# Kernel tuning notes

Hardware: AMD Instinct MI355X
Metric: run time of the kernel (lower is better)

Reference implementation:

```python
import jax, jax.numpy as jnp
import numpy as np

B, D, K, V = 8192, 64, 200, 100000
EPS = 1e-5


def setup_inputs() -> dict:
    key = jax.random.key(0)
    ks = jax.random.split(key, 16)
    n = lambda k, s, sc=1.0: jax.random.normal(k, s, dtype=jnp.float32) * sc
    sw = 0.05  # weight scale for numeric stability
    inp = {
        'v_embed': n(ks[0], (V, D)),
        'embeds_u_1': n(ks[1], (B, D)),
        'embeds_u_2': n(ks[2], (B, D)),
        'embeds_u_3': n(ks[3], (B, D)),
        'embeds_u_4': n(ks[4], (B, D)),
        'embeds_v': n(ks[5], (B, D)),
        'w_ur1_w': n(ks[6], (D, D), sw), 'w_ur1_b': jnp.zeros((D,), jnp.float32),
        'w_ur2_w': n(ks[7], (D, D), sw), 'w_ur2_b': jnp.zeros((D,), jnp.float32),
        'w_vr1_w': n(ks[8], (D, D), sw), 'w_vr1_b': jnp.zeros((D,), jnp.float32),
        'w_vr2_w': n(ks[9], (D, D), sw), 'w_vr2_b': jnp.zeros((D,), jnp.float32),
        'w_uv1_w': n(ks[10], (2 * D, D), sw), 'w_uv1_b': jnp.zeros((D,), jnp.float32),
        'w_uv2_w': n(ks[11], (D, 16), sw), 'w_uv2_b': jnp.zeros((16,), jnp.float32),
        'w_uv3_w': n(ks[12], (16, 1), sw), 'w_uv3_b': jnp.zeros((1,), jnp.float32),
        'nodes_v': jax.random.randint(ks[13], (B,), 0, V),
        'nbr_idx': jax.random.randint(ks[14], (B, K), 0, V),
        'nbr_len': jax.random.randint(ks[15], (B,), 1, K),
    }
    for name, dim in (('bn1', D), ('bn2', D), ('bn3', D), ('bn4', 16)):
        inp[name + '_g'] = jnp.ones((dim,), jnp.float32)
        inp[name + '_b'] = jnp.zeros((dim,), jnp.float32)
        inp[name + '_m'] = jnp.zeros((dim,), jnp.float32)
        inp[name + '_v'] = jnp.ones((dim,), jnp.float32)
    return inp


def _bn(x, g, b, m, v):
    return (x - m) * jax.lax.rsqrt(v + EPS) * g + b


def reference(v_embed, embeds_u_1, embeds_u_2, embeds_u_3, embeds_u_4, embeds_v,
              w_ur1_w, w_ur1_b, w_ur2_w, w_ur2_b,
              w_vr1_w, w_vr1_b, w_vr2_w, w_vr2_b,
              w_uv1_w, w_uv1_b, w_uv2_w, w_uv2_b, w_uv3_w, w_uv3_b,
              bn1_g, bn1_b, bn1_m, bn1_v,
              bn2_g, bn2_b, bn2_m, bn2_v,
              bn3_g, bn3_b, bn3_m, bn3_v,
              bn4_g, bn4_b, bn4_m, bn4_v,
              nodes_v, nbr_idx, nbr_len):
    sg = jax.lax.stop_gradient
    # ragged nearest-neighbor min distance (torch used .data -> detached)
    ve = sg(v_embed)
    new_v = ve[nodes_v]                                    # [B, D]
    nbr = ve[nbr_idx]                                      # [B, K, D]
    d = jnp.sqrt(jnp.sum((new_v[:, None, :] - nbr) ** 2, axis=-1))  # [B, K]
    kk = nbr_idx.shape[1]
    mask = jnp.arange(kk)[None, :] < jnp.maximum(nbr_len, 1)[:, None]
    d_min = jnp.min(jnp.where(mask, d, jnp.inf), axis=1)   # [B]
    # per-sample curiosity c_u (detached in torch via .data)
    dist = lambda a, b: jnp.sqrt(jnp.sum((a - b) ** 2, axis=-1))
    u1, u2, u3, u4 = sg(embeds_u_1), sg(embeds_u_2), sg(embeds_u_3), sg(embeds_u_4)
    c = (dist(u1, u2) + dist(u2, u3) + dist(u3, u4)) / 3.0  # [B]
    # exponential-decay fusion of temporal user embeddings: e^-4..e^-1 / sum
    w = jnp.exp(-jnp.arange(4, 0, -1, dtype=jnp.float32))
    w = w / jnp.sum(w)
    embeds_u = (embeds_u_1 * w[0] + embeds_u_2 * w[1]
                + embeds_u_3 * w[2] + embeds_u_4 * w[3])
    # MLP head (eval mode: BN with running stats, dropout off)
    x_u = jax.nn.relu(_bn(embeds_u @ w_ur1_w + w_ur1_b, bn1_g, bn1_b, bn1_m, bn1_v))
    x_u = x_u @ w_ur2_w + w_ur2_b
    x_v = jax.nn.relu(_bn(embeds_v @ w_vr1_w + w_vr1_b, bn2_g, bn2_b, bn2_m, bn2_v))
    x_v = x_v @ w_vr2_w + w_vr2_b
    x = jnp.concatenate([x_u, x_v], axis=1)                # [B, 2D]
    x = jax.nn.relu(_bn(x @ w_uv1_w + w_uv1_b, bn3_g, bn3_b, bn3_m, bn3_v))
    x = jax.nn.relu(_bn(x @ w_uv2_w + w_uv2_b, bn4_g, bn4_b, bn4_m, bn4_v))
    scores = (x @ w_uv3_w + w_uv3_b)[:, 0]                 # [B]
    # unexpectedness term: batch min-max normalize, 6t*exp(-6t)
    t = (d_min - jnp.min(d_min)) / (jnp.max(d_min) - jnp.min(d_min))
    unexp = 6.0 * t * jnp.exp(-6.0 * t)
    cn = (c - jnp.min(c)) / (jnp.max(c) - jnp.min(c))
    return scores + unexp * cn
```

## Files before the change

kernel.cpp:

```cpp
#include <hip/hip_runtime.h>
#include <math.h>

#define NROWS 8192
#define DIM 64
#define KNBR 200
#define NSLICE 8
#define SLICE_ROWS 12500
#define RPB 32
#define BN_EPS 1e-5f
#define BIGF 3.402823466e38f


__device__ __forceinline__ float matvec64(const float* xlds,
                                          const float* __restrict__ W,
                                          int lane) {
    float acc = 0.f;
#pragma unroll
    for (int i4 = 0; i4 < 16; ++i4) {
        float4 xv = *(const float4*)(xlds + i4 * 4);
        acc = fmaf(xv.x, W[(i4 * 4 + 0) * 64 + lane], acc);
        acc = fmaf(xv.y, W[(i4 * 4 + 1) * 64 + lane], acc);
        acc = fmaf(xv.z, W[(i4 * 4 + 2) * 64 + lane], acc);
        acc = fmaf(xv.w, W[(i4 * 4 + 3) * 64 + lane], acc);
    }
    return acc;
}

__device__ __forceinline__ float matvec128(const float* xlds,
                                           const float* __restrict__ W,
                                           int lane) {
    float acc = 0.f;
#pragma unroll
    for (int i4 = 0; i4 < 32; ++i4) {
        float4 xv = *(const float4*)(xlds + i4 * 4);
        acc = fmaf(xv.x, W[(i4 * 4 + 0) * 64 + lane], acc);
        acc = fmaf(xv.y, W[(i4 * 4 + 1) * 64 + lane], acc);
        acc = fmaf(xv.z, W[(i4 * 4 + 2) * 64 + lane], acc);
        acc = fmaf(xv.w, W[(i4 * 4 + 3) * 64 + lane], acc);
    }
    return acc;
}

__device__ __forceinline__ float d2part(const float4 a, const float4 b) {
    const float dx = a.x - b.x, dy = a.y - b.y, dz = a.z - b.z, dw = a.w - b.w;
    float d2 = dx * dx;
    d2 = fmaf(dy, dy, d2);
    d2 = fmaf(dz, dz, d2);
    d2 = fmaf(dw, dw, d2);
    return d2;
}

__global__ __launch_bounds__(256) void bin_rows(
    const float* __restrict__ v_embed,
    const int* __restrict__ nodes_v,
    const int* __restrict__ nbr_idx, const int* __restrict__ nbr_len,
    int* __restrict__ ws_list, int* __restrict__ ws_cnt,
    int* __restrict__ ws_off, float* __restrict__ ws_q) {
    const int w = threadIdx.x >> 6;
    const int lane = threadIdx.x & 63;
    const int row = blockIdx.x * 4 + w;

    __shared__ int cnt[4][NSLICE];
    __shared__ int off[4][NSLICE];

    if (lane < NSLICE) cnt[w][lane] = 0;
    __syncthreads();

    const int node = nodes_v[row];
    if (lane < 16) {
        const float4 vq = ((const float4*)(v_embed + ((size_t)node << 6)))[lane];
        ((float4*)(ws_q + (size_t)row * DIM))[lane] = vq;
    }

    int len = nbr_len[row];
    if (len < 1) len = 1;
    const int* nb = nbr_idx + (size_t)row * KNBR;

    int myidx[4], myslice[4], mypos[4];
#pragma unroll
    for (int t = 0; t < 4; ++t) {
        const int k = t * 64 + lane;
        const bool v = k < len;
        const int idx = v ? nb[k] : 0;
        const int s = idx / SLICE_ROWS;
        myidx[t] = idx;
        myslice[t] = s;
        mypos[t] = v ? atomicAdd(&cnt[w][s], 1) : 0;
    }
    __syncthreads();
    if (lane == 0) {
        int acc = 0;
#pragma unroll
        for (int s = 0; s < NSLICE; ++s) { off[w][s] = acc; acc += cnt[w][s]; }
    }
    __syncthreads();
#pragma unroll
    for (int t = 0; t < 4; ++t) {
        const int k = t * 64 + lane;
        if (k < len) {
            ws_list[(size_t)row * KNBR + off[w][myslice[t]] + mypos[t]] = myidx[t];
        }
    }
    if (lane < NSLICE) {
        ws_cnt[row * NSLICE + lane] = cnt[w][lane];
        ws_off[row * NSLICE + lane] = off[w][lane];
    }
}

#define GATHER_BLOCKS (NROWS / RPB * NSLICE)
__global__ __launch_bounds__(256) void fused_main(
    const float* __restrict__ v_embed,
    const float* __restrict__ u1p, const float* __restrict__ u2p,
    const float* __restrict__ u3p, const float* __restrict__ u4p,
    const float* __restrict__ evp,
    const float* __restrict__ w_ur1, const float* __restrict__ b_ur1,
    const float* __restrict__ w_ur2, const float* __restrict__ b_ur2,
    const float* __restrict__ w_vr1, const float* __restrict__ b_vr1,
    const float* __restrict__ w_vr2, const float* __restrict__ b_vr2,
    const float* __restrict__ w_uv1, const float* __restrict__ b_uv1,
    const float* __restrict__ w_uv2, const float* __restrict__ b_uv2,
    const float* __restrict__ w_uv3, const float* __restrict__ b_uv3,
    const float* __restrict__ bn1_g, const float* __restrict__ bn1_b,
    const float* __restrict__ bn1_m, const float* __restrict__ bn1_v,
    const float* __restrict__ bn2_g, const float* __restrict__ bn2_b,
    const float* __restrict__ bn2_m, const float* __restrict__ bn2_v,
    const float* __restrict__ bn3_g, const float* __restrict__ bn3_b,
    const float* __restrict__ bn3_m, const float* __restrict__ bn3_v,
    const float* __restrict__ bn4_g, const float* __restrict__ bn4_b,
    const float* __restrict__ bn4_m, const float* __restrict__ bn4_v,
    const int* __restrict__ ws_list, const int* __restrict__ ws_cnt,
    const int* __restrict__ ws_off, const float* __restrict__ ws_q,
    float* __restrict__ out_score, float* __restrict__ ws_d2p,
    float* __restrict__ ws_c) {
    const int w = threadIdx.x >> 6;
    const int lane = threadIdx.x & 63;

    __shared__ float xbuf[4][132];
    __shared__ int scnt[RPB];
    __shared__ int soff[RPB];

    if (blockIdx.x < GATHER_BLOCKS) {
        const int s = blockIdx.x & 7;
        const int rgroup = blockIdx.x >> 3;
        const int row0 = rgroup * RPB;

        if (threadIdx.x < RPB) {
            scnt[threadIdx.x] = ws_cnt[(row0 + threadIdx.x) * NSLICE + s];
            soff[threadIdx.x] = ws_off[(row0 + threadIdx.x) * NSLICE + s];
        }
        __syncthreads();

        const int riq = lane >> 4;
        const int slot = (lane >> 2) & 3;
        const int sub = lane & 3;

#pragma unroll
        for (int qg = 0; qg < 2; ++qg) {
            const int lr = w * 8 + qg * 4 + riq;
            const int row = row0 + lr;
            const int cnt = scnt[lr];
            float dmin2 = BIGF;
            if (cnt > 0) {
                const int off = soff[lr];
                const float4* qr = (const float4*)(ws_q + (size_t)row * DIM);
                const float4 q0 = qr[sub + 0];
                const float4 q1 = qr[sub + 4];
                const float4 q2 = qr[sub + 8];
                const float4 q3 = qr[sub + 12];
                const int* lst = ws_list + (size_t)row * KNBR + off;
                const int cm1 = cnt - 1;
                for (int j0 = 0; j0 < cnt; j0 += 4) {
                    int j = j0 + slot;
                    j = j < cm1 ? j : cm1;
                    const int idx = lst[j];
                    const float4* r = (const float4*)(v_embed + ((size_t)idx << 6));
                    const float4 a0 = r[sub + 0];
                    const float4 a1 = r[sub + 4];
                    const float4 a2 = r[sub + 8];
                    const float4 a3 = r[sub + 12];
                    float d = d2part(q0, a0) + d2part(q1, a1)
                            + d2part(q2, a2) + d2part(q3, a3);
                    d += __shfl_xor(d, 1);
                    d += __shfl_xor(d, 2);
                    dmin2 = fminf(dmin2, d);
                }
            }
            dmin2 = fminf(dmin2, __shfl_xor(dmin2, 4));
            dmin2 = fminf(dmin2, __shfl_xor(dmin2, 8));
            if ((lane & 15) == 0) ws_d2p[row * NSLICE + s] = dmin2;
        }
        return;
    }

    const int row = (blockIdx.x - GATHER_BLOCKS) * 4 + w;
    float* xw = xbuf[w];
    const size_t rb = (size_t)row * DIM + lane;
    const float u1 = u1p[rb], u2 = u2p[rb], u3 = u3p[rb], u4 = u4p[rb];
    const float ev = evp[rb];

    float d12 = u1 - u2, d23 = u2 - u3, d34 = u3 - u4;
    float s1 = d12 * d12, s2 = d23 * d23, s3 = d34 * d34;
#pragma unroll
    for (int m = 1; m < 64; m <<= 1) {
        s1 += __shfl_xor(s1, m);
        s2 += __shfl_xor(s2, m);
        s3 += __shfl_xor(s3, m);
    }
    const float cval = (sqrtf(s1) + sqrtf(s2) + sqrtf(s3)) * (1.0f / 3.0f);

    float eu = u1 * 0.032058603280084993f;
    eu = fmaf(u2, 0.087144318742032567f, eu);
    eu = fmaf(u3, 0.236882818089910134f, eu);
    eu = fmaf(u4, 0.643914259887972245f, eu);

    xw[lane] = eu;
    float t1 = matvec64(xw, w_ur1, lane) + b_ur1[lane];
    t1 = (t1 - bn1_m[lane]) * rsqrtf(bn1_v[lane] + BN_EPS) * bn1_g[lane] + bn1_b[lane];
    t1 = fmaxf(t1, 0.f);
    xw[lane] = t1;
    const float xu = matvec64(xw, w_ur2, lane) + b_ur2[lane];
    xw[lane] = ev;
    float t2 = matvec64(xw, w_vr1, lane) + b_vr1[lane];
    t2 = (t2 - bn2_m[lane]) * rsqrtf(bn2_v[lane] + BN_EPS) * bn2_g[lane] + bn2_b[lane];
    t2 = fmaxf(t2, 0.f);
    xw[lane] = t2;
    const float xv = matvec64(xw, w_vr2, lane) + b_vr2[lane];
    xw[lane] = xu;
    xw[64 + lane] = xv;
    float t3 = matvec128(xw, w_uv1, lane) + b_uv1[lane];
    t3 = (t3 - bn3_m[lane]) * rsqrtf(bn3_v[lane] + BN_EPS) * bn3_g[lane] + bn3_b[lane];
    t3 = fmaxf(t3, 0.f);
    xw[lane] = t3;
    const int jj = lane & 15;
    const int q = lane >> 4;
    float h4 = 0.f;
#pragma unroll
    for (int i = 0; i < 16; ++i) {
        h4 = fmaf(xw[q * 16 + i], w_uv2[(q * 16 + i) * 16 + jj], h4);
    }
    h4 += __shfl_xor(h4, 16);
    h4 += __shfl_xor(h4, 32);
    h4 += b_uv2[jj];
    h4 = (h4 - bn4_m[jj]) * rsqrtf(bn4_v[jj] + BN_EPS) * bn4_g[jj] + bn4_b[jj];
    h4 = fmaxf(h4, 0.f);
    float p = h4 * w_uv3[jj];
#pragma unroll
    for (int m = 1; m < 16; m <<= 1) p += __shfl_xor(p, m);
    const float score = p + b_uv3[0];

    if (lane == 0) {
        out_score[row] = score;
        ws_c[row] = cval;
    }
}

__global__ __launch_bounds__(1024) void combine(
    const float* __restrict__ ws_d2p, const float* __restrict__ ws_c,
    float* __restrict__ out) {
    const int tid = threadIdx.x;
    __shared__ float red[4][16];

    float ld2[8], lc[8];
    float dmin = BIGF, dmax = -BIGF, cmin = BIGF, cmax = -BIGF;
#pragma unroll
    for (int i = 0; i < 8; ++i) {
        const int b = tid * 8 + i;
        float m = ws_d2p[b * NSLICE];
#pragma unroll
        for (int s = 1; s < NSLICE; ++s) m = fminf(m, ws_d2p[b * NSLICE + s]);
        ld2[i] = m;
        lc[i] = ws_c[b];
        dmin = fminf(dmin, m);
        dmax = fmaxf(dmax, m);
        cmin = fminf(cmin, lc[i]);
        cmax = fmaxf(cmax, lc[i]);
    }
#pragma unroll
    for (int m = 1; m < 64; m <<= 1) {
        dmin = fminf(dmin, __shfl_xor(dmin, m));
        dmax = fmaxf(dmax, __shfl_xor(dmax, m));
        cmin = fminf(cmin, __shfl_xor(cmin, m));
        cmax = fmaxf(cmax, __shfl_xor(cmax, m));
    }
    const int wid = tid >> 6;
    const int lane = tid & 63;
    if (lane == 0) {
        red[0][wid] = dmin;
        red[1][wid] = dmax;
        red[2][wid] = cmin;
        red[3][wid] = cmax;
    }
    __syncthreads();
    dmin = red[0][0]; dmax = red[1][0]; cmin = red[2][0]; cmax = red[3][0];
#pragma unroll
    for (int i = 1; i < 16; ++i) {
        dmin = fminf(dmin, red[0][i]);
        dmax = fmaxf(dmax, red[1][i]);
        cmin = fminf(cmin, red[2][i]);
        cmax = fmaxf(cmax, red[3][i]);
    }
    const float dlo = sqrtf(dmin);
    const float dhi = sqrtf(dmax);
    const float inv_d = 1.f / (dhi - dlo);
    const float inv_c = 1.f / (cmax - cmin);
#pragma unroll
    for (int i = 0; i < 8; ++i) {
        const int b = tid * 8 + i;
        const float t = (sqrtf(ld2[i]) - dlo) * inv_d;
        const float unexp = 6.f * t * expf(-6.f * t);
        out[b] += unexp * (lc[i] - cmin) * inv_c;
    }
}

extern "C" void kernel_launch(void* const* d_in, const int* in_sizes, int n_in,
                              void* d_out, int out_size, void* d_ws, size_t ws_size,
                              hipStream_t stream) {
    const float* v_embed = (const float*)d_in[0];
    const float* u1 = (const float*)d_in[1];
    const float* u2 = (const float*)d_in[2];
    const float* u3 = (const float*)d_in[3];
    const float* u4 = (const float*)d_in[4];
    const float* ev = (const float*)d_in[5];
    const float* w_ur1 = (const float*)d_in[6];
    const float* b_ur1 = (const float*)d_in[7];
    const float* w_ur2 = (const float*)d_in[8];
    const float* b_ur2 = (const float*)d_in[9];
    const float* w_vr1 = (const float*)d_in[10];
    const float* b_vr1 = (const float*)d_in[11];
    const float* w_vr2 = (const float*)d_in[12];
    const float* b_vr2 = (const float*)d_in[13];
    const float* w_uv1 = (const float*)d_in[14];
    const float* b_uv1 = (const float*)d_in[15];
    const float* w_uv2 = (const float*)d_in[16];
    const float* b_uv2 = (const float*)d_in[17];
    const float* w_uv3 = (const float*)d_in[18];
    const float* b_uv3 = (const float*)d_in[19];
    const int* nodes_v = (const int*)d_in[20];
    const int* nbr_idx = (const int*)d_in[21];
    const int* nbr_len = (const int*)d_in[22];
    const float* bn1_g = (const float*)d_in[23];
    const float* bn1_b = (const float*)d_in[24];
    const float* bn1_m = (const float*)d_in[25];
    const float* bn1_v = (const float*)d_in[26];
    const float* bn2_g = (const float*)d_in[27];
    const float* bn2_b = (const float*)d_in[28];
    const float* bn2_m = (const float*)d_in[29];
    const float* bn2_v = (const float*)d_in[30];
    const float* bn3_g = (const float*)d_in[31];
    const float* bn3_b = (const float*)d_in[32];
    const float* bn3_m = (const float*)d_in[33];
    const float* bn3_v = (const float*)d_in[34];
    const float* bn4_g = (const float*)d_in[35];
    const float* bn4_b = (const float*)d_in[36];
    const float* bn4_m = (const float*)d_in[37];
    const float* bn4_v = (const float*)d_in[38];

    float* out = (float*)d_out;
    int* ws_list = (int*)d_ws;
    int* ws_cnt = ws_list + (size_t)NROWS * KNBR;
    int* ws_off = ws_cnt + NROWS * NSLICE;
    float* ws_d2p = (float*)(ws_off + NROWS * NSLICE);
    float* ws_c = ws_d2p + NROWS * NSLICE;
    float* ws_q = ws_c + NROWS;

    hipLaunchKernelGGL(bin_rows, dim3(NROWS / 4), dim3(256), 0, stream,
                       v_embed, nodes_v, nbr_idx, nbr_len,
                       ws_list, ws_cnt, ws_off, ws_q);
    hipLaunchKernelGGL(fused_main, dim3(GATHER_BLOCKS + NROWS / 4), dim3(256), 0, stream,
                       v_embed, u1, u2, u3, u4, ev,
                       w_ur1, b_ur1, w_ur2, b_ur2, w_vr1, b_vr1, w_vr2, b_vr2,
                       w_uv1, b_uv1, w_uv2, b_uv2, w_uv3, b_uv3,
                       bn1_g, bn1_b, bn1_m, bn1_v,
                       bn2_g, bn2_b, bn2_m, bn2_v,
                       bn3_g, bn3_b, bn3_m, bn3_v,
                       bn4_g, bn4_b, bn4_m, bn4_v,
                       ws_list, ws_cnt, ws_off, ws_q,
                       out, ws_d2p, ws_c);
    hipLaunchKernelGGL(combine, dim3(1), dim3(1024), 0, stream,
                       ws_d2p, ws_c, out);
}
```

Before: 70.22 us.

## Batch MLP rows per wave, fold BN constants, reorder blocks, unroll gather by two

The MLP path now processes 8 rows per wave, so each weight element loaded from global memory is reused across 8 rows held in shared memory instead of being reloaded per row. Bias and eval-mode batch-norm are folded into one scale and offset per column, computed once. MLP blocks are placed before the gather blocks in the grid so they are scheduled first and overlap with the gather work, and the gather loop handles two neighbours per slot per iteration to keep more loads in flight. This adds register pressure from the eight accumulators and the doubled gather loads, and leaves fewer MLP blocks (256 instead of 2048).

```diff
diff --git a/kernel.cpp b/kernel.cpp
--- a/kernel.cpp
+++ b/kernel.cpp
@@ -7,39 +7,11 @@
 #define NSLICE 8
 #define SLICE_ROWS 12500
 #define RPB 32
+#define MROWS 8
+#define MLP_BLOCKS 256
+#define GATHER_BLOCKS (NROWS / RPB * NSLICE)
 #define BN_EPS 1e-5f
 #define BIGF 3.402823466e38f
-
-
-__device__ __forceinline__ float matvec64(const float* xlds,
-                                          const float* __restrict__ W,
-                                          int lane) {
-    float acc = 0.f;
-#pragma unroll
-    for (int i4 = 0; i4 < 16; ++i4) {
-        float4 xv = *(const float4*)(xlds + i4 * 4);
-        acc = fmaf(xv.x, W[(i4 * 4 + 0) * 64 + lane], acc);
-        acc = fmaf(xv.y, W[(i4 * 4 + 1) * 64 + lane], acc);
-        acc = fmaf(xv.z, W[(i4 * 4 + 2) * 64 + lane], acc);
-        acc = fmaf(xv.w, W[(i4 * 4 + 3) * 64 + lane], acc);
-    }
-    return acc;
-}
-
-__device__ __forceinline__ float matvec128(const float* xlds,
-                                           const float* __restrict__ W,
-                                           int lane) {
-    float acc = 0.f;
-#pragma unroll
-    for (int i4 = 0; i4 < 32; ++i4) {
-        float4 xv = *(const float4*)(xlds + i4 * 4);
-        acc = fmaf(xv.x, W[(i4 * 4 + 0) * 64 + lane], acc);
-        acc = fmaf(xv.y, W[(i4 * 4 + 1) * 64 + lane], acc);
-        acc = fmaf(xv.z, W[(i4 * 4 + 2) * 64 + lane], acc);
-        acc = fmaf(xv.w, W[(i4 * 4 + 3) * 64 + lane], acc);
-    }
-    return acc;
-}
 
 __device__ __forceinline__ float d2part(const float4 a, const float4 b) {
     const float dx = a.x - b.x, dy = a.y - b.y, dz = a.z - b.z, dw = a.w - b.w;
@@ -48,6 +20,27 @@
     d2 = fmaf(dz, dz, d2);
     d2 = fmaf(dw, dw, d2);
     return d2;
+}
+
+__device__ __forceinline__ void mv8(const float* X, int xoff,
+                                    const float* __restrict__ W,
+                                    int lane, float* acc, int in4) {
+#pragma unroll
+    for (int r = 0; r < MROWS; ++r) acc[r] = 0.f;
+    for (int i4 = 0; i4 < in4; ++i4) {
+        const float w0 = W[(i4 * 4 + 0) * 64 + lane];
+        const float w1 = W[(i4 * 4 + 1) * 64 + lane];
+        const float w2 = W[(i4 * 4 + 2) * 64 + lane];
+        const float w3 = W[(i4 * 4 + 3) * 64 + lane];
+#pragma unroll
+        for (int r = 0; r < MROWS; ++r) {
+            const float4 xv = *(const float4*)&X[r * 132 + xoff + i4 * 4];
+            acc[r] = fmaf(xv.x, w0, acc[r]);
+            acc[r] = fmaf(xv.y, w1, acc[r]);
+            acc[r] = fmaf(xv.z, w2, acc[r]);
+            acc[r] = fmaf(xv.w, w3, acc[r]);
+        }
+    }
 }
 
 __global__ __launch_bounds__(256) void bin_rows(
@@ -107,7 +100,6 @@
     }
 }
 
-#define GATHER_BLOCKS (NROWS / RPB * NSLICE)
 __global__ __launch_bounds__(256) void fused_main(
     const float* __restrict__ v_embed,
     const float* __restrict__ u1p, const float* __restrict__ u2p,
@@ -135,14 +127,14 @@
     const int w = threadIdx.x >> 6;
     const int lane = threadIdx.x & 63;
 
-    __shared__ float xbuf[4][132];
+    __shared__ float xsbuf[4][MROWS][132];
     __shared__ int scnt[RPB];
     __shared__ int soff[RPB];
 
-    if (blockIdx.x < GATHER_BLOCKS) {
-        const int s = blockIdx.x & 7;
-        const int rgroup = blockIdx.x >> 3;
-        const int row0 = rgroup * RPB;
+    if (blockIdx.x >= MLP_BLOCKS) {
+        const int gb = blockIdx.x - MLP_BLOCKS;
+        const int s = gb & 7;
+        const int row0 = (gb >> 3) * RPB;
 
         if (threadIdx.x < RPB) {
             scnt[threadIdx.x] = ws_cnt[(row0 + threadIdx.x) * NSLICE + s];
@@ -169,20 +161,24 @@
                 const float4 q3 = qr[sub + 12];
                 const int* lst = ws_list + (size_t)row * KNBR + off;
                 const int cm1 = cnt - 1;
-                for (int j0 = 0; j0 < cnt; j0 += 4) {
-                    int j = j0 + slot;
-                    j = j < cm1 ? j : cm1;
-                    const int idx = lst[j];
-                    const float4* r = (const float4*)(v_embed + ((size_t)idx << 6));
-                    const float4 a0 = r[sub + 0];
-                    const float4 a1 = r[sub + 4];
-                    const float4 a2 = r[sub + 8];
-                    const float4 a3 = r[sub + 12];
-                    float d = d2part(q0, a0) + d2part(q1, a1)
-                            + d2part(q2, a2) + d2part(q3, a3);
-                    d += __shfl_xor(d, 1);
-                    d += __shfl_xor(d, 2);
-                    dmin2 = fminf(dmin2, d);
+                for (int j0 = 0; j0 < cnt; j0 += 8) {
+                    int ja = j0 + slot;        ja = ja < cm1 ? ja : cm1;
+                    int jb = j0 + 4 + slot;    jb = jb < cm1 ? jb : cm1;
+                    const int ia = lst[ja];
+                    const int ib = lst[jb];
+                    const float4* ra = (const float4*)(v_embed + ((size_t)ia << 6));
+                    const float4* rb = (const float4*)(v_embed + ((size_t)ib << 6));
+                    const float4 a0 = ra[sub + 0], a1 = ra[sub + 4];
+                    const float4 a2 = ra[sub + 8], a3 = ra[sub + 12];
+                    const float4 c0 = rb[sub + 0], c1 = rb[sub + 4];
+                    const float4 c2 = rb[sub + 8], c3 = rb[sub + 12];
+                    float da = d2part(q0, a0) + d2part(q1, a1)
+                             + d2part(q2, a2) + d2part(q3, a3);
+                    float db = d2part(q0, c0) + d2part(q1, c1)
+                             + d2part(q2, c2) + d2part(q3, c3);
+                    da += __shfl_xor(da, 1); da += __shfl_xor(da, 2);
+                    db += __shfl_xor(db, 1); db += __shfl_xor(db, 2);
+                    dmin2 = fminf(dmin2, fminf(da, db));
                 }
             }
             dmin2 = fminf(dmin2, __shfl_xor(dmin2, 4));
@@ -192,65 +188,102 @@
         return;
     }
 
-    const int row = (blockIdx.x - GATHER_BLOCKS) * 4 + w;
-    float* xw = xbuf[w];
-    const size_t rb = (size_t)row * DIM + lane;
-    const float u1 = u1p[rb], u2 = u2p[rb], u3 = u3p[rb], u4 = u4p[rb];
-    const float ev = evp[rb];
-
-    float d12 = u1 - u2, d23 = u2 - u3, d34 = u3 - u4;
-    float s1 = d12 * d12, s2 = d23 * d23, s3 = d34 * d34;
-#pragma unroll
-    for (int m = 1; m < 64; m <<= 1) {
-        s1 += __shfl_xor(s1, m);
-        s2 += __shfl_xor(s2, m);
-        s3 += __shfl_xor(s3, m);
-    }
-    const float cval = (sqrtf(s1) + sqrtf(s2) + sqrtf(s3)) * (1.0f / 3.0f);
-
-    float eu = u1 * 0.032058603280084993f;
-    eu = fmaf(u2, 0.087144318742032567f, eu);
-    eu = fmaf(u3, 0.236882818089910134f, eu);
-    eu = fmaf(u4, 0.643914259887972245f, eu);
-
-    xw[lane] = eu;
-    float t1 = matvec64(xw, w_ur1, lane) + b_ur1[lane];
-    t1 = (t1 - bn1_m[lane]) * rsqrtf(bn1_v[lane] + BN_EPS) * bn1_g[lane] + bn1_b[lane];
-    t1 = fmaxf(t1, 0.f);
-    xw[lane] = t1;
-    const float xu = matvec64(xw, w_ur2, lane) + b_ur2[lane];
-    xw[lane] = ev;
-    float t2 = matvec64(xw, w_vr1, lane) + b_vr1[lane];
-    t2 = (t2 - bn2_m[lane]) * rsqrtf(bn2_v[lane] + BN_EPS) * bn2_g[lane] + bn2_b[lane];
-    t2 = fmaxf(t2, 0.f);
-    xw[lane] = t2;
-    const float xv = matvec64(xw, w_vr2, lane) + b_vr2[lane];
-    xw[lane] = xu;
-    xw[64 + lane] = xv;
-    float t3 = matvec128(xw, w_uv1, lane) + b_uv1[lane];
-    t3 = (t3 - bn3_m[lane]) * rsqrtf(bn3_v[lane] + BN_EPS) * bn3_g[lane] + bn3_b[lane];
-    t3 = fmaxf(t3, 0.f);
-    xw[lane] = t3;
-    const int jj = lane & 15;
+    const int mrow0 = (blockIdx.x * 4 + w) * MROWS;
+    float* X = &xsbuf[w][0][0];
+
+    const float s1v = rsqrtf(bn1_v[lane] + BN_EPS) * bn1_g[lane];
+    const float o1v = bn1_b[lane] + (b_ur1[lane] - bn1_m[lane]) * s1v;
+    const float s2v = rsqrtf(bn2_v[lane] + BN_EPS) * bn2_g[lane];
+    const float o2v = bn2_b[lane] + (b_vr1[lane] - bn2_m[lane]) * s2v;
+    const float s3v = rsqrtf(bn3_v[lane] + BN_EPS) * bn3_g[lane];
+    const float o3v = bn3_b[lane] + (b_uv1[lane] - bn3_m[lane]) * s3v;
+    const int col = lane & 15;
     const int q = lane >> 4;
-    float h4 = 0.f;
-#pragma unroll
-    for (int i = 0; i < 16; ++i) {
-        h4 = fmaf(xw[q * 16 + i], w_uv2[(q * 16 + i) * 16 + jj], h4);
-    }
-    h4 += __shfl_xor(h4, 16);
-    h4 += __shfl_xor(h4, 32);
-    h4 += b_uv2[jj];
-    h4 = (h4 - bn4_m[jj]) * rsqrtf(bn4_v[jj] + BN_EPS) * bn4_g[jj] + bn4_b[jj];
-    h4 = fmaxf(h4, 0.f);
-    float p = h4 * w_uv3[jj];
-#pragma unroll
-    for (int m = 1; m < 16; m <<= 1) p += __shfl_xor(p, m);
-    const float score = p + b_uv3[0];
-
-    if (lane == 0) {
-        out_score[row] = score;
-        ws_c[row] = cval;
+    const float s4v = rsqrtf(bn4_v[col] + BN_EPS) * bn4_g[col];
+    const float o4v = bn4_b[col] + (b_uv2[col] - bn4_m[col]) * s4v;
+    const float w3c = w_uv3[col];
+    const float b3 = b_uv3[0];
+    const float bu2 = b_ur2[lane];
+    const float bv2 = b_vr2[lane];
+
+#pragma unroll 2
+    for (int r = 0; r < MROWS; ++r) {
+        const int row = mrow0 + r;
+        const size_t rb = (size_t)row * DIM + lane;
+        const float u1 = u1p[rb], u2 = u2p[rb], u3 = u3p[rb], u4 = u4p[rb];
+        const float ev = evp[rb];
+        float d12 = u1 - u2, d23 = u2 - u3, d34 = u3 - u4;
+        float s1 = d12 * d12, s2 = d23 * d23, s3 = d34 * d34;
+#pragma unroll
+        for (int m = 1; m < 64; m <<= 1) {
+            s1 += __shfl_xor(s1, m);
+            s2 += __shfl_xor(s2, m);
+            s3 += __shfl_xor(s3, m);
+        }
+        if (lane == 0) {
+            ws_c[row] = (sqrtf(s1) + sqrtf(s2) + sqrtf(s3)) * (1.0f / 3.0f);
+        }
+        float eu = u1 * 0.032058603280084993f;
+        eu = fmaf(u2, 0.087144318742032567f, eu);
+        eu = fmaf(u3, 0.236882818089910134f, eu);
+        eu = fmaf(u4, 0.643914259887972245f, eu);
+        X[r * 132 + lane] = eu;
+        X[r * 132 + 64 + lane] = ev;
+    }
+
+    float acc[MROWS];
+    mv8(X, 64, w_vr1, lane, acc, 16);
+#pragma unroll
+    for (int r = 0; r < MROWS; ++r)
+        X[r * 132 + 64 + lane] = fmaxf(fmaf(acc[r], s2v, o2v), 0.f);
+    mv8(X, 64, w_vr2, lane, acc, 16);
+#pragma unroll
+    for (int r = 0; r < MROWS; ++r)
+        X[r * 132 + 64 + lane] = acc[r] + bv2;
+    mv8(X, 0, w_ur1, lane, acc, 16);
+#pragma unroll
+    for (int r = 0; r < MROWS; ++r)
+        X[r * 132 + lane] = fmaxf(fmaf(acc[r], s1v, o1v), 0.f);
+    mv8(X, 0, w_ur2, lane, acc, 16);
+#pragma unroll
+    for (int r = 0; r < MROWS; ++r)
+        X[r * 132 + lane] = acc[r] + bu2;
+    mv8(X, 0, w_uv1, lane, acc, 32);
+#pragma unroll
+    for (int r = 0; r < MROWS; ++r)
+        X[r * 132 + lane] = fmaxf(fmaf(acc[r], s3v, o3v), 0.f);
+
+    float acc2[MROWS];
+#pragma unroll
+    for (int r = 0; r < MROWS; ++r) acc2[r] = 0.f;
+#pragma unroll
+    for (int i4 = 0; i4 < 4; ++i4) {
+        const int ii = q * 16 + i4 * 4;
+        const float v0 = w_uv2[(ii + 0) * 16 + col];
+        const float v1 = w_uv2[(ii + 1) * 16 + col];
+        const float v2 = w_uv2[(ii + 2) * 16 + col];
+        const float v3 = w_uv2[(ii + 3) * 16 + col];
+#pragma unroll
+        for (int r = 0; r < MROWS; ++r) {
+            const float4 xv = *(const float4*)&X[r * 132 + ii];
+            acc2[r] = fmaf(xv.x, v0, acc2[r]);
+            acc2[r] = fmaf(xv.y, v1, acc2[r]);
+            acc2[r] = fmaf(xv.z, v2, acc2[r]);
+            acc2[r] = fmaf(xv.w, v3, acc2[r]);
+        }
+    }
+#pragma unroll
+    for (int r = 0; r < MROWS; ++r) {
+        float a = acc2[r];
+        a += __shfl_xor(a, 16);
+        a += __shfl_xor(a, 32);
+        const float h = fmaxf(fmaf(a, s4v, o4v), 0.f);
+        float p = h * w3c;
+        p += __shfl_xor(p, 1);
+        p += __shfl_xor(p, 2);
+        p += __shfl_xor(p, 4);
+        p += __shfl_xor(p, 8);
+        if (lane == 0) out_score[mrow0 + r] = p + b3;
     }
 }
 
@@ -366,7 +399,7 @@
     hipLaunchKernelGGL(bin_rows, dim3(NROWS / 4), dim3(256), 0, stream,
                        v_embed, nodes_v, nbr_idx, nbr_len,
                        ws_list, ws_cnt, ws_off, ws_q);
-    hipLaunchKernelGGL(fused_main, dim3(GATHER_BLOCKS + NROWS / 4), dim3(256), 0, stream,
+    hipLaunchKernelGGL(fused_main, dim3(MLP_BLOCKS + GATHER_BLOCKS), dim3(256), 0, stream,
                        v_embed, u1, u2, u3, u4, ev,
                        w_ur1, b_ur1, w_ur2, b_ur2, w_vr1, b_vr1, w_vr2, b_vr2,
                        w_uv1, b_uv1, w_uv2, b_uv2, w_uv3, b_uv3,
```

Result: no change. 71.57 us (+1.9%).
